# Kernel optimization log

Measured on AMD Instinct MI355X. Metric: run time of the kernel, lower is better.

Reference implementation:

```python
import jax, jax.numpy as jnp
import numpy as np

N_PER_DEG = 30000
MAX_DEG = 6
MIN_DEG = 0
N_ATOMS = N_PER_DEG * (MAX_DEG + 1)  # 210000, atoms sorted by degree
N_FEAT = 128
NB_FILTER = 128
NB_AFFINE = 2 * MAX_DEG + (1 - MIN_DEG)  # 13


def setup_inputs() -> dict:
    key = jax.random.key(0)
    ks = jax.random.split(key, 2 + MAX_DEG)
    atoms = jax.random.normal(ks[0], (N_ATOMS, N_FEAT), dtype=jnp.float32)
    # glorot-ish scale for the 13 affine weights
    W = jax.random.normal(ks[1], (NB_AFFINE, N_FEAT, NB_FILTER), dtype=jnp.float32) * (1.0 / np.sqrt(N_FEAT))
    b = jnp.zeros((NB_AFFINE, NB_FILTER), dtype=jnp.float32)
    # deg_slice[d] = (start, count) for degree d in 0..MAX_DEG; equal-size buckets
    deg_slice = jnp.asarray(
        np.stack([np.arange(MAX_DEG + 1) * N_PER_DEG,
                  np.full(MAX_DEG + 1, N_PER_DEG)], axis=1).astype(np.int32))
    inp = {"atoms": atoms, "W": W, "b": b, "deg_slice": deg_slice}
    for d in range(1, MAX_DEG + 1):
        inp[f"adj{d}"] = jax.random.randint(ks[1 + d], (N_PER_DEG, d), 0, N_ATOMS, dtype=jnp.int32)
    return inp


def reference(atoms, W, b, deg_slice, adj1, adj2, adj3, adj4, adj5, adj6):
    """Degree-bucketed graph convolution (deepchem GraphConv, linear activation).

    W ordering matches the original iterator: for deg=1..MAX_DEG the pair
    (rel=W[2*(deg-1)], self=W[2*(deg-1)+1]), then deg-0 self uses W[2*MAX_DEG].
    Output concat order: deg 0 bucket first, then deg 1..MAX_DEG.
    """
    adjs = [adj1, adj2, adj3, adj4, adj5, adj6]
    ds = np.asarray(deg_slice)  # structural constant: static slice bounds
    outs = [None] * (MAX_DEG + 1 - MIN_DEG)
    # deg 0: self-affine only
    s0, c0 = int(ds[0, 0]), int(ds[0, 1])
    outs[0] = atoms[s0:s0 + c0] @ W[2 * MAX_DEG] + b[2 * MAX_DEG]
    for deg in range(1, MAX_DEG + 1):
        s, c = int(ds[deg, 0]), int(ds[deg, 1])
        # gather neighbors of each degree-deg atom and sum: (c, deg, F) -> (c, F)
        rel = jnp.take(atoms, adjs[deg - 1], axis=0).sum(axis=1)
        out = (rel @ W[2 * (deg - 1)] + b[2 * (deg - 1)]
               + atoms[s:s + c] @ W[2 * (deg - 1) + 1] + b[2 * (deg - 1) + 1])
        outs[deg] = out
    return jnp.concatenate(outs, axis=0)  # (N_ATOMS, NB_FILTER)
```

## Files before the change

kernel.cpp:

```cpp
#include <hip/hip_runtime.h>
#include <hip/hip_bf16.h>

#define NPD 30000
#define NF  128
#define MAXDEG 6
#define LDK 136

typedef __attribute__((ext_vector_type(8))) short short8;
typedef __attribute__((ext_vector_type(4))) float floatx4;

__device__ __forceinline__ float bf2f(unsigned short u) {
    unsigned v = ((unsigned)u) << 16; return __builtin_bit_cast(float, v);
}
__device__ __forceinline__ unsigned short f2bf(float f) {
    __hip_bfloat16 h = __float2bfloat16(f);
    return __builtin_bit_cast(unsigned short, h);
}

__global__ void sniff_kernel(const unsigned* __restrict__ w, int* __restrict__ flag) {
    __shared__ int cnt[256];
    int c = 0;
#pragma unroll
    for (int i = 0; i < 4; i++) {
        unsigned x = w[threadIdx.x * 4 + i];
        unsigned e = (x >> 7) & 0xFFu;
        c += (e >= 100u && e <= 131u) ? 1 : 0;
    }
    cnt[threadIdx.x] = c;
    __syncthreads();
    if (threadIdx.x == 0) {
        int s = 0;
        for (int i = 0; i < 256; i++) s += cnt[i];
        flag[0] = (s < 614) ? 1 : 0;
    }
}

__global__ __launch_bounds__(256, 2) void gconv_kernel(
    const void* __restrict__ atoms_,
    const void* __restrict__ W_,
    const void* __restrict__ b_,
    const int* __restrict__ adj1, const int* __restrict__ adj2,
    const int* __restrict__ adj3, const int* __restrict__ adj4,
    const int* __restrict__ adj5, const int* __restrict__ adj6,
    const int* __restrict__ flag,
    void* __restrict__ out_)
{
    __shared__ unsigned short sA[128 * LDK];

    const int isf32 = flag[0];
    const float*          atomsF = (const float*)atoms_;
    const unsigned short* atomsH = (const unsigned short*)atoms_;

    const int tid  = threadIdx.x;
    const int lane = tid & 63;
    const int wave = tid >> 6;
    const int wr   = wave >> 1, wc = wave & 1;
    const int deg  = blockIdx.y;
    const int row0_local = blockIdx.x * 128;
    const int valid = min(128, NPD - row0_local);
    const int row0g = deg * NPD + row0_local;

    floatx4 acc[4][4];
#pragma unroll
    for (int i = 0; i < 4; i++)
#pragma unroll
        for (int j = 0; j < 4; j++) acc[i][j] = (floatx4){0.f, 0.f, 0.f, 0.f};

    const int nb = lane & 15;
    const int kq = (lane >> 4) * 8;

    auto run_phase = [&](int wi) {
        const float*          WF = (const float*)W_ + (size_t)wi * NF * NF;
        const unsigned short* WH = (const unsigned short*)W_ + (size_t)wi * NF * NF;
        short8 bfr[4][4];
#pragma unroll
        for (int kk = 0; kk < 4; ++kk) {
#pragma unroll
            for (int nt = 0; nt < 4; ++nt) {
                const int n = wc * 64 + nt * 16 + nb;
                const int kb = kk * 32 + kq;
                short8 f;
                if (isf32) {
#pragma unroll
                    for (int j = 0; j < 8; ++j)
                        f[j] = (short)f2bf(WF[(size_t)(kb + j) * NF + n]);
                } else {
#pragma unroll
                    for (int j = 0; j < 8; ++j)
                        f[j] = (short)WH[(size_t)(kb + j) * NF + n];
                }
                bfr[kk][nt] = f;
            }
        }
#pragma unroll
        for (int kk = 0; kk < 4; ++kk) {
            short8 af[4];
#pragma unroll
            for (int mt = 0; mt < 4; ++mt)
                af[mt] = *(const short8*)(&sA[(wr * 64 + mt * 16 + nb) * LDK + kk * 32 + kq]);
#pragma unroll
            for (int mt = 0; mt < 4; ++mt)
#pragma unroll
                for (int nt = 0; nt < 4; ++nt)
                    acc[mt][nt] = __builtin_amdgcn_mfma_f32_16x16x32_bf16(
                        af[mt], bfr[kk][nt], acc[mt][nt], 0, 0, 0);
        }
    };

#pragma unroll
    for (int p = 0; p < 8; p++) {
        int idx = p * 256 + tid;
        int r  = idx >> 4;
        int kc = (idx & 15) << 3;
        int rr = min(r, valid - 1);
        size_t off = (size_t)(row0g + rr) * NF + kc;
        uint4 v;
        if (isf32) {
            const float4* pf = (const float4*)(atomsF + off);
            float4 f0 = pf[0], f1 = pf[1];
            unsigned w0 = (unsigned)f2bf(f0.x) | ((unsigned)f2bf(f0.y) << 16);
            unsigned w1 = (unsigned)f2bf(f0.z) | ((unsigned)f2bf(f0.w) << 16);
            unsigned w2 = (unsigned)f2bf(f1.x) | ((unsigned)f2bf(f1.y) << 16);
            unsigned w3 = (unsigned)f2bf(f1.z) | ((unsigned)f2bf(f1.w) << 16);
            v = (uint4){w0, w1, w2, w3};
        } else {
            v = *(const uint4*)(atomsH + off);
        }
        *(uint4*)(&sA[r * LDK + kc]) = v;
    }
    const int wi_self = (deg == 0) ? 12 : (2 * deg - 1);
    __syncthreads();
    run_phase(wi_self);

    if (deg > 0) {
        const int* adj = (deg == 1) ? adj1 : (deg == 2) ? adj2 : (deg == 3) ? adj3
                        : (deg == 4) ? adj4 : (deg == 5) ? adj5 : adj6;
        __syncthreads();
#pragma unroll
        for (int p = 0; p < 4; p++) {
            int idx = p * 256 + tid;
            int r  = idx >> 3;
            int kc = (idx & 7) << 4;
            int rr = min(r, valid - 1);
            const int* arow = adj + (size_t)(row0_local + rr) * deg;
            float a16[16];
#pragma unroll
            for (int i = 0; i < 16; i++) a16[i] = 0.f;
            for (int j = 0; j < deg; j++) {
                size_t off = (size_t)arow[j] * NF + kc;
                if (isf32) {
                    const float4* pf = (const float4*)(atomsF + off);
                    float4 q0 = pf[0], q1 = pf[1], q2 = pf[2], q3 = pf[3];
                    a16[0]  += q0.x; a16[1]  += q0.y; a16[2]  += q0.z; a16[3]  += q0.w;
                    a16[4]  += q1.x; a16[5]  += q1.y; a16[6]  += q1.z; a16[7]  += q1.w;
                    a16[8]  += q2.x; a16[9]  += q2.y; a16[10] += q2.z; a16[11] += q2.w;
                    a16[12] += q3.x; a16[13] += q3.y; a16[14] += q3.z; a16[15] += q3.w;
                } else {
                    const uint4* ph = (const uint4*)(atomsH + off);
                    uint4 v0 = ph[0], v1 = ph[1];
                    a16[0]  += bf2f((unsigned short)(v0.x)); a16[1]  += bf2f((unsigned short)(v0.x >> 16));
                    a16[2]  += bf2f((unsigned short)(v0.y)); a16[3]  += bf2f((unsigned short)(v0.y >> 16));
                    a16[4]  += bf2f((unsigned short)(v0.z)); a16[5]  += bf2f((unsigned short)(v0.z >> 16));
                    a16[6]  += bf2f((unsigned short)(v0.w)); a16[7]  += bf2f((unsigned short)(v0.w >> 16));
                    a16[8]  += bf2f((unsigned short)(v1.x)); a16[9]  += bf2f((unsigned short)(v1.x >> 16));
                    a16[10] += bf2f((unsigned short)(v1.y)); a16[11] += bf2f((unsigned short)(v1.y >> 16));
                    a16[12] += bf2f((unsigned short)(v1.z)); a16[13] += bf2f((unsigned short)(v1.z >> 16));
                    a16[14] += bf2f((unsigned short)(v1.w)); a16[15] += bf2f((unsigned short)(v1.w >> 16));
                }
            }
            unsigned ww[8];
#pragma unroll
            for (int i = 0; i < 8; i++) {
                unsigned lo = f2bf(a16[2 * i]);
                unsigned hi = f2bf(a16[2 * i + 1]);
                ww[i] = lo | (hi << 16);
            }
            *(uint4*)(&sA[r * LDK + kc])     = *(uint4*)&ww[0];
            *(uint4*)(&sA[r * LDK + kc + 8]) = *(uint4*)&ww[4];
        }
        __syncthreads();
        run_phase(2 * (deg - 1));
    }

    const float*          BF = (const float*)b_;
    const unsigned short* BH = (const unsigned short*)b_;
    float bias[4];
#pragma unroll
    for (int nt = 0; nt < 4; nt++) {
        int n = wc * 64 + nt * 16 + nb;
        float bv = isf32 ? BF[wi_self * NF + n] : bf2f(BH[wi_self * NF + n]);
        if (deg > 0)
            bv += isf32 ? BF[(2 * (deg - 1)) * NF + n] : bf2f(BH[(2 * (deg - 1)) * NF + n]);
        bias[nt] = bv;
    }
    const int rq = (lane >> 4) << 2;
#pragma unroll
    for (int mt = 0; mt < 4; mt++) {
        int rb = wr * 64 + mt * 16 + rq;
#pragma unroll
        for (int reg = 0; reg < 4; reg++) {
            int r = rb + reg;
            if (r < valid) {
                size_t rowoff = (size_t)(row0g + r) * NF;
                if (isf32) {
                    float* op = (float*)out_ + rowoff;
#pragma unroll
                    for (int nt = 0; nt < 4; nt++) {
                        int n = wc * 64 + nt * 16 + nb;
                        op[n] = acc[mt][nt][reg] + bias[nt];
                    }
                } else {
                    unsigned short* op = (unsigned short*)out_ + rowoff;
#pragma unroll
                    for (int nt = 0; nt < 4; nt++) {
                        int n = wc * 64 + nt * 16 + nb;
                        op[n] = f2bf(acc[mt][nt][reg] + bias[nt]);
                    }
                }
            }
        }
    }
}

extern "C" void kernel_launch(void* const* d_in, const int* in_sizes, int n_in,
                              void* d_out, int out_size, void* d_ws, size_t ws_size,
                              hipStream_t stream) {
    const void* atoms = d_in[0];
    const void* W     = d_in[1];
    const void* b     = d_in[2];
    const int* adj1 = (const int*)d_in[4];
    const int* adj2 = (const int*)d_in[5];
    const int* adj3 = (const int*)d_in[6];
    const int* adj4 = (const int*)d_in[7];
    const int* adj5 = (const int*)d_in[8];
    const int* adj6 = (const int*)d_in[9];
    int* flag = (int*)d_ws;

    sniff_kernel<<<1, 256, 0, stream>>>((const unsigned*)atoms, flag);
    gconv_kernel<<<dim3((NPD + 127) / 128, MAXDEG + 1), 256, 0, stream>>>(
        atoms, W, b, adj1, adj2, adj3, adj4, adj5, adj6, flag, d_out);
}
```

Measured before the change: 277.6 us.

## Pretranspose weights to bf16, halve row tile, unroll templated neighbor gather

Drops the dtype-sniff kernel and the bf16 input path so the kernel assumes fp32 inputs throughout. A small pre-kernel now converts and transposes the 13 weight matrices into bf16 in the workspace, which lets the B fragments load as contiguous 16-byte vectors instead of strided scalar reads. The row tile shrinks from 128 to 64, doubling the block count and cutting accumulator registers. The neighbor gather is templated on degree with fully unrolled index and row loads, so each thread handles 32 features with more loads in flight. This adds a second launch and relies on the workspace being large enough, falling back to the old strided weight loads otherwise.

```diff
diff --git a/kernel.cpp b/kernel.cpp
--- a/kernel.cpp
+++ b/kernel.cpp
@@ -4,65 +4,81 @@
 #define NPD 30000
 #define NF  128
 #define MAXDEG 6
+#define TM  64
 #define LDK 136
 
 typedef __attribute__((ext_vector_type(8))) short short8;
 typedef __attribute__((ext_vector_type(4))) float floatx4;
 
-__device__ __forceinline__ float bf2f(unsigned short u) {
-    unsigned v = ((unsigned)u) << 16; return __builtin_bit_cast(float, v);
-}
 __device__ __forceinline__ unsigned short f2bf(float f) {
     __hip_bfloat16 h = __float2bfloat16(f);
     return __builtin_bit_cast(unsigned short, h);
 }
 
-__global__ void sniff_kernel(const unsigned* __restrict__ w, int* __restrict__ flag) {
-    __shared__ int cnt[256];
-    int c = 0;
-#pragma unroll
-    for (int i = 0; i < 4; i++) {
-        unsigned x = w[threadIdx.x * 4 + i];
-        unsigned e = (x >> 7) & 0xFFu;
-        c += (e >= 100u && e <= 131u) ? 1 : 0;
-    }
-    cnt[threadIdx.x] = c;
+__global__ void wt_kernel(const float* __restrict__ W,
+                          unsigned short* __restrict__ Wt) {
+    __shared__ unsigned short t[32][33];
+    const int a  = blockIdx.z;
+    const int k0 = blockIdx.x * 32, n0 = blockIdx.y * 32;
+    const int tx = threadIdx.x & 31, ty = threadIdx.x >> 5;
+    const float*    Wp  = W  + (size_t)a * NF * NF;
+    unsigned short* Wtp = Wt + (size_t)a * NF * NF;
+#pragma unroll
+    for (int i = 0; i < 32; i += 8)
+        t[ty + i][tx] = f2bf(Wp[(size_t)(k0 + ty + i) * NF + (n0 + tx)]);
     __syncthreads();
-    if (threadIdx.x == 0) {
-        int s = 0;
-        for (int i = 0; i < 256; i++) s += cnt[i];
-        flag[0] = (s < 614) ? 1 : 0;
-    }
-}
-
-__global__ __launch_bounds__(256, 2) void gconv_kernel(
-    const void* __restrict__ atoms_,
-    const void* __restrict__ W_,
-    const void* __restrict__ b_,
+#pragma unroll
+    for (int i = 0; i < 32; i += 8)
+        Wtp[(size_t)(n0 + ty + i) * NF + (k0 + tx)] = t[tx][ty + i];
+}
+
+template <int DEG>
+__device__ __forceinline__ void gather_sum(const int* __restrict__ adj,
+                                           const float* __restrict__ atoms,
+                                           int row_glob, int kc, float* a32) {
+    const int* arow = adj + (size_t)row_glob * DEG;
+    int idxs[DEG];
+#pragma unroll
+    for (int j = 0; j < DEG; j++) idxs[j] = arow[j];
+#pragma unroll
+    for (int i = 0; i < 32; i++) a32[i] = 0.f;
+#pragma unroll
+    for (int j = 0; j < DEG; j++) {
+        const float4* p = (const float4*)(atoms + (size_t)idxs[j] * NF + kc);
+#pragma unroll
+        for (int q = 0; q < 8; q++) {
+            float4 v = p[q];
+            a32[q * 4 + 0] += v.x; a32[q * 4 + 1] += v.y;
+            a32[q * 4 + 2] += v.z; a32[q * 4 + 3] += v.w;
+        }
+    }
+}
+
+__global__ __launch_bounds__(256) void gconv_kernel(
+    const float* __restrict__ atoms,
+    const float* __restrict__ W,
+    const unsigned short* __restrict__ Wt,
+    const float* __restrict__ bvec,
     const int* __restrict__ adj1, const int* __restrict__ adj2,
     const int* __restrict__ adj3, const int* __restrict__ adj4,
     const int* __restrict__ adj5, const int* __restrict__ adj6,
-    const int* __restrict__ flag,
-    void* __restrict__ out_)
+    const int use_wt,
+    float* __restrict__ out)
 {
-    __shared__ unsigned short sA[128 * LDK];
-
-    const int isf32 = flag[0];
-    const float*          atomsF = (const float*)atoms_;
-    const unsigned short* atomsH = (const unsigned short*)atoms_;
+    __shared__ unsigned short sA[TM * LDK];
 
     const int tid  = threadIdx.x;
     const int lane = tid & 63;
     const int wave = tid >> 6;
     const int wr   = wave >> 1, wc = wave & 1;
     const int deg  = blockIdx.y;
-    const int row0_local = blockIdx.x * 128;
-    const int valid = min(128, NPD - row0_local);
+    const int row0_local = blockIdx.x * TM;
+    const int valid = min(TM, NPD - row0_local);
     const int row0g = deg * NPD + row0_local;
 
-    floatx4 acc[4][4];
-#pragma unroll
-    for (int i = 0; i < 4; i++)
+    floatx4 acc[2][4];
+#pragma unroll
+    for (int i = 0; i < 2; i++)
 #pragma unroll
         for (int j = 0; j < 4; j++) acc[i][j] = (floatx4){0.f, 0.f, 0.f, 0.f};
 
@@ -70,152 +86,105 @@
     const int kq = (lane >> 4) * 8;
 
     auto run_phase = [&](int wi) {
-        const float*          WF = (const float*)W_ + (size_t)wi * NF * NF;
-        const unsigned short* WH = (const unsigned short*)W_ + (size_t)wi * NF * NF;
-        short8 bfr[4][4];
+        const unsigned short* Wtp = Wt + (size_t)wi * NF * NF;
+        const float*          Wfp = W  + (size_t)wi * NF * NF;
 #pragma unroll
         for (int kk = 0; kk < 4; ++kk) {
-#pragma unroll
-            for (int nt = 0; nt < 4; ++nt) {
-                const int n = wc * 64 + nt * 16 + nb;
-                const int kb = kk * 32 + kq;
-                short8 f;
-                if (isf32) {
+            short8 bfr[4];
+            if (use_wt) {
+#pragma unroll
+                for (int nt = 0; nt < 4; ++nt)
+                    bfr[nt] = *(const short8*)(Wtp + (size_t)(wc * 64 + nt * 16 + nb) * NF
+                                               + kk * 32 + kq);
+            } else {
+#pragma unroll
+                for (int nt = 0; nt < 4; ++nt) {
+                    short8 f;
 #pragma unroll
                     for (int j = 0; j < 8; ++j)
-                        f[j] = (short)f2bf(WF[(size_t)(kb + j) * NF + n]);
-                } else {
-#pragma unroll
-                    for (int j = 0; j < 8; ++j)
-                        f[j] = (short)WH[(size_t)(kb + j) * NF + n];
+                        f[j] = (short)f2bf(Wfp[(size_t)(kk * 32 + kq + j) * NF
+                                               + (wc * 64 + nt * 16 + nb)]);
+                    bfr[nt] = f;
                 }
-                bfr[kk][nt] = f;
             }
-        }
-#pragma unroll
-        for (int kk = 0; kk < 4; ++kk) {
-            short8 af[4];
-#pragma unroll
-            for (int mt = 0; mt < 4; ++mt)
-                af[mt] = *(const short8*)(&sA[(wr * 64 + mt * 16 + nb) * LDK + kk * 32 + kq]);
-#pragma unroll
-            for (int mt = 0; mt < 4; ++mt)
+            short8 af[2];
+#pragma unroll
+            for (int mt = 0; mt < 2; ++mt)
+                af[mt] = *(const short8*)(&sA[(wr * 32 + mt * 16 + nb) * LDK + kk * 32 + kq]);
+#pragma unroll
+            for (int mt = 0; mt < 2; ++mt)
 #pragma unroll
                 for (int nt = 0; nt < 4; ++nt)
                     acc[mt][nt] = __builtin_amdgcn_mfma_f32_16x16x32_bf16(
-                        af[mt], bfr[kk][nt], acc[mt][nt], 0, 0, 0);
+                        af[mt], bfr[nt], acc[mt][nt], 0, 0, 0);
         }
     };
 
-#pragma unroll
-    for (int p = 0; p < 8; p++) {
-        int idx = p * 256 + tid;
-        int r  = idx >> 4;
-        int kc = (idx & 15) << 3;
-        int rr = min(r, valid - 1);
-        size_t off = (size_t)(row0g + rr) * NF + kc;
-        uint4 v;
-        if (isf32) {
-            const float4* pf = (const float4*)(atomsF + off);
-            float4 f0 = pf[0], f1 = pf[1];
-            unsigned w0 = (unsigned)f2bf(f0.x) | ((unsigned)f2bf(f0.y) << 16);
-            unsigned w1 = (unsigned)f2bf(f0.z) | ((unsigned)f2bf(f0.w) << 16);
-            unsigned w2 = (unsigned)f2bf(f1.x) | ((unsigned)f2bf(f1.y) << 16);
-            unsigned w3 = (unsigned)f2bf(f1.z) | ((unsigned)f2bf(f1.w) << 16);
-            v = (uint4){w0, w1, w2, w3};
-        } else {
-            v = *(const uint4*)(atomsH + off);
-        }
-        *(uint4*)(&sA[r * LDK + kc]) = v;
+    const int rS  = tid >> 2;
+    const int kcS = (tid & 3) << 5;
+    const int rrS = min(rS, valid - 1);
+
+    {
+        const float4* p = (const float4*)(atoms + (size_t)(row0g + rrS) * NF + kcS);
+        unsigned ww[16];
+#pragma unroll
+        for (int q = 0; q < 8; q++) {
+            float4 v = p[q];
+            ww[q * 2 + 0] = (unsigned)f2bf(v.x) | ((unsigned)f2bf(v.y) << 16);
+            ww[q * 2 + 1] = (unsigned)f2bf(v.z) | ((unsigned)f2bf(v.w) << 16);
+        }
+#pragma unroll
+        for (int s = 0; s < 4; s++)
+            *(uint4*)(&sA[rS * LDK + kcS + s * 8]) = *(uint4*)&ww[s * 4];
     }
     const int wi_self = (deg == 0) ? 12 : (2 * deg - 1);
     __syncthreads();
     run_phase(wi_self);
 
     if (deg > 0) {
-        const int* adj = (deg == 1) ? adj1 : (deg == 2) ? adj2 : (deg == 3) ? adj3
-                        : (deg == 4) ? adj4 : (deg == 5) ? adj5 : adj6;
         __syncthreads();
-#pragma unroll
-        for (int p = 0; p < 4; p++) {
-            int idx = p * 256 + tid;
-            int r  = idx >> 3;
-            int kc = (idx & 7) << 4;
-            int rr = min(r, valid - 1);
-            const int* arow = adj + (size_t)(row0_local + rr) * deg;
-            float a16[16];
-#pragma unroll
-            for (int i = 0; i < 16; i++) a16[i] = 0.f;
-            for (int j = 0; j < deg; j++) {
-                size_t off = (size_t)arow[j] * NF + kc;
-                if (isf32) {
-                    const float4* pf = (const float4*)(atomsF + off);
-                    float4 q0 = pf[0], q1 = pf[1], q2 = pf[2], q3 = pf[3];
-                    a16[0]  += q0.x; a16[1]  += q0.y; a16[2]  += q0.z; a16[3]  += q0.w;
-                    a16[4]  += q1.x; a16[5]  += q1.y; a16[6]  += q1.z; a16[7]  += q1.w;
-                    a16[8]  += q2.x; a16[9]  += q2.y; a16[10] += q2.z; a16[11] += q2.w;
-                    a16[12] += q3.x; a16[13] += q3.y; a16[14] += q3.z; a16[15] += q3.w;
-                } else {
-                    const uint4* ph = (const uint4*)(atomsH + off);
-                    uint4 v0 = ph[0], v1 = ph[1];
-                    a16[0]  += bf2f((unsigned short)(v0.x)); a16[1]  += bf2f((unsigned short)(v0.x >> 16));
-                    a16[2]  += bf2f((unsigned short)(v0.y)); a16[3]  += bf2f((unsigned short)(v0.y >> 16));
-                    a16[4]  += bf2f((unsigned short)(v0.z)); a16[5]  += bf2f((unsigned short)(v0.z >> 16));
-                    a16[6]  += bf2f((unsigned short)(v0.w)); a16[7]  += bf2f((unsigned short)(v0.w >> 16));
-                    a16[8]  += bf2f((unsigned short)(v1.x)); a16[9]  += bf2f((unsigned short)(v1.x >> 16));
-                    a16[10] += bf2f((unsigned short)(v1.y)); a16[11] += bf2f((unsigned short)(v1.y >> 16));
-                    a16[12] += bf2f((unsigned short)(v1.z)); a16[13] += bf2f((unsigned short)(v1.z >> 16));
-                    a16[14] += bf2f((unsigned short)(v1.w)); a16[15] += bf2f((unsigned short)(v1.w >> 16));
-                }
-            }
-            unsigned ww[8];
-#pragma unroll
-            for (int i = 0; i < 8; i++) {
-                unsigned lo = f2bf(a16[2 * i]);
-                unsigned hi = f2bf(a16[2 * i + 1]);
-                ww[i] = lo | (hi << 16);
-            }
-            *(uint4*)(&sA[r * LDK + kc])     = *(uint4*)&ww[0];
-            *(uint4*)(&sA[r * LDK + kc + 8]) = *(uint4*)&ww[4];
-        }
+        float a32[32];
+        const int rg = row0_local + rrS;
+        switch (deg) {
+            case 1: gather_sum<1>(adj1, atoms, rg, kcS, a32); break;
+            case 2: gather_sum<2>(adj2, atoms, rg, kcS, a32); break;
+            case 3: gather_sum<3>(adj3, atoms, rg, kcS, a32); break;
+            case 4: gather_sum<4>(adj4, atoms, rg, kcS, a32); break;
+            case 5: gather_sum<5>(adj5, atoms, rg, kcS, a32); break;
+            default: gather_sum<6>(adj6, atoms, rg, kcS, a32); break;
+        }
+        unsigned ww[16];
+#pragma unroll
+        for (int i = 0; i < 16; i++)
+            ww[i] = (unsigned)f2bf(a32[2 * i]) | ((unsigned)f2bf(a32[2 * i + 1]) << 16);
+#pragma unroll
+        for (int s = 0; s < 4; s++)
+            *(uint4*)(&sA[rS * LDK + kcS + s * 8]) = *(uint4*)&ww[s * 4];
         __syncthreads();
         run_phase(2 * (deg - 1));
     }
 
-    const float*          BF = (const float*)b_;
-    const unsigned short* BH = (const unsigned short*)b_;
     float bias[4];
 #pragma unroll
     for (int nt = 0; nt < 4; nt++) {
         int n = wc * 64 + nt * 16 + nb;
-        float bv = isf32 ? BF[wi_self * NF + n] : bf2f(BH[wi_self * NF + n]);
-        if (deg > 0)
-            bv += isf32 ? BF[(2 * (deg - 1)) * NF + n] : bf2f(BH[(2 * (deg - 1)) * NF + n]);
+        float bv = bvec[wi_self * NF + n];
+        if (deg > 0) bv += bvec[(2 * (deg - 1)) * NF + n];
         bias[nt] = bv;
     }
     const int rq = (lane >> 4) << 2;
 #pragma unroll
-    for (int mt = 0; mt < 4; mt++) {
-        int rb = wr * 64 + mt * 16 + rq;
+    for (int mt = 0; mt < 2; mt++) {
+        int rb = wr * 32 + mt * 16 + rq;
 #pragma unroll
         for (int reg = 0; reg < 4; reg++) {
             int r = rb + reg;
             if (r < valid) {
-                size_t rowoff = (size_t)(row0g + r) * NF;
-                if (isf32) {
-                    float* op = (float*)out_ + rowoff;
-#pragma unroll
-                    for (int nt = 0; nt < 4; nt++) {
-                        int n = wc * 64 + nt * 16 + nb;
-                        op[n] = acc[mt][nt][reg] + bias[nt];
-                    }
-                } else {
-                    unsigned short* op = (unsigned short*)out_ + rowoff;
-#pragma unroll
-                    for (int nt = 0; nt < 4; nt++) {
-                        int n = wc * 64 + nt * 16 + nb;
-                        op[n] = f2bf(acc[mt][nt][reg] + bias[nt]);
-                    }
+                float* op = out + (size_t)(row0g + r) * NF;
+#pragma unroll
+                for (int nt = 0; nt < 4; nt++) {
+                    int n = wc * 64 + nt * 16 + nb;
+                    op[n] = acc[mt][nt][reg] + bias[nt];
                 }
             }
         }
@@ -225,18 +194,23 @@
 extern "C" void kernel_launch(void* const* d_in, const int* in_sizes, int n_in,
                               void* d_out, int out_size, void* d_ws, size_t ws_size,
                               hipStream_t stream) {
-    const void* atoms = d_in[0];
-    const void* W     = d_in[1];
-    const void* b     = d_in[2];
+    const float* atoms = (const float*)d_in[0];
+    const float* W     = (const float*)d_in[1];
+    const float* b     = (const float*)d_in[2];
     const int* adj1 = (const int*)d_in[4];
     const int* adj2 = (const int*)d_in[5];
     const int* adj3 = (const int*)d_in[6];
     const int* adj4 = (const int*)d_in[7];
     const int* adj5 = (const int*)d_in[8];
     const int* adj6 = (const int*)d_in[9];
-    int* flag = (int*)d_ws;
-
-    sniff_kernel<<<1, 256, 0, stream>>>((const unsigned*)atoms, flag);
-    gconv_kernel<<<dim3((NPD + 127) / 128, MAXDEG + 1), 256, 0, stream>>>(
-        atoms, W, b, adj1, adj2, adj3, adj4, adj5, adj6, flag, d_out);
-}
+
+    const size_t wt_bytes = (size_t)13 * NF * NF * sizeof(unsigned short);
+    const int use_wt = (ws_size >= wt_bytes) ? 1 : 0;
+    unsigned short* Wt = (unsigned short*)d_ws;
+
+    if (use_wt)
+        wt_kernel<<<dim3(4, 4, 13), 256, 0, stream>>>(W, Wt);
+    gconv_kernel<<<dim3((NPD + TM - 1) / TM, MAXDEG + 1), 256, 0, stream>>>(
+        atoms, W, Wt, b, adj1, adj2, adj3, adj4, adj5, adj6, use_wt,
+        (float*)d_out);
+}
```

Result: slower. 291.8 us (+5.1%).
